# Kernel optimization log

Hardware: AMD Instinct MI355X
Metric: run time of the kernel (lower is better)

Reference implementation:

```python
import jax, jax.numpy as jnp
import numpy as np
import math

B, C, N, L = 32, 128, 2048, 1
H, DK, APT = 8, 16, 10
EPS = 1e-5


def conv1x1(x, W, b):
    # 1x1 Conv2d on [B, C, N, L]
    return jnp.einsum('oc,bcnl->bonl', W, x) + b[None, :, None, None]


def layer_norm_12(x):
    # normalize over dims (1, 2) as in the custom LayerNorm (no affine)
    mean = x.mean(axis=(1, 2), keepdims=True)
    var = x.var(axis=(1, 2), keepdims=True)
    return (x - mean) / jnp.sqrt(var + EPS)


def setup_inputs() -> dict:
    key = jax.random.key(0)
    ks = jax.random.split(key, 10)
    s = 0.05  # small-scale init for numerical stability
    inp = {
        'input': jax.random.normal(ks[0], (B, C, N, L), jnp.float32),
        'Wq': jax.random.normal(ks[1], (C, C), jnp.float32) * s,
        'bq': jnp.zeros((C,), jnp.float32),
        'Wv': jax.random.normal(ks[2], (C, C), jnp.float32) * s,
        'bv': jnp.zeros((C,), jnp.float32),
        'Wc': jax.random.normal(ks[3], (C, C), jnp.float32) * s,
        'bc': jnp.zeros((C,), jnp.float32),
        'memory': jax.random.normal(ks[4], (H, L, N, DK), jnp.float32) * s,
        'sa_weight': jnp.ones((C, N, L), jnp.float32),
        'sa_bias': jnp.zeros((C, N, L), jnp.float32),
        'nodevec1': jax.random.normal(ks[5], (N, APT), jnp.float32),
        'nodevec2': jax.random.normal(ks[6], (APT, N), jnp.float32),
        'Wg1': jax.random.normal(ks[7], (C, C), jnp.float32) * s,
        'bg1': jnp.zeros((C,), jnp.float32),
        'Wg2': jax.random.normal(ks[8], (C, C), jnp.float32) * s,
        'bg2': jnp.zeros((C,), jnp.float32),
        'Wg3': jax.random.normal(ks[9], (C, C), jnp.float32) * s,
        'bg3': jnp.zeros((C,), jnp.float32),
    }
    return inp


def reference(input, Wq, bq, Wv, bv, Wc, bc, memory, sa_weight, sa_bias,
              nodevec1, nodevec2, Wg1, bg1, Wg2, bg2, Wg3, bg3):
    scale = math.sqrt(DK)

    def split_heads(t):  # [B,C,N,L] -> [B,H,L,N,DK]
        return t.reshape(B, H, DK, N, L).transpose(0, 1, 4, 3, 2)

    # SpatialAttention (Conv = 1x1 conv + relu; dropout off in eval)
    q = jax.nn.relu(conv1x1(input, Wq, bq))
    v = jax.nn.relu(conv1x1(input, Wv, bv))
    query = jax.nn.softmax(split_heads(q) / scale, axis=-1)     # [B,H,L,N,DK]
    value = split_heads(v)                                       # [B,H,L,N,DK]
    key = jax.nn.softmax(memory / scale, axis=-1)                # [H,L,N,DK]
    Aapt = jax.nn.softmax(jax.nn.relu(nodevec1 @ nodevec2), axis=-1)  # [N,N]

    kv = jnp.einsum('hlnx,bhlny->bhlxy', key, value)             # [B,H,L,DK,DK]
    attn_qkv = jnp.einsum('bhlnx,bhlxy->bhlny', query, kv)       # [B,H,L,N,DK]
    attn_dyn = jnp.einsum('nm,bhlnc->bhlnc', Aapt, value)        # row-sum scaling
    x = attn_qkv + attn_dyn

    # merge heads back to [B,C,N,L] and apply concat conv (Conv = conv+relu)
    x = x.transpose(0, 1, 4, 3, 2).reshape(B, C, N, L)
    x = jax.nn.relu(conv1x1(x, Wc, bc))
    x = x * sa_weight[None] + sa_bias[None] + x                  # affine branch

    # Encoder wrap
    x = x + input
    x = layer_norm_12(x)
    g = conv1x1(x, Wg1, bg1) * jax.nn.sigmoid(conv1x1(x, Wg2, bg2))
    g = conv1x1(g, Wg3, bg3)                                     # GLU
    x = g + x
    x = x * sa_weight[None] + sa_bias[None] + x
    x = layer_norm_12(x)
    return x
```

## Files before the change

kernel.cpp:

```cpp
#include <hip/hip_runtime.h>
#include <hip/hip_bf16.h>
#include <math.h>

#define DI __device__ __forceinline__

typedef short bf16x8 __attribute__((ext_vector_type(8)));
typedef float f32x4 __attribute__((ext_vector_type(4)));

constexpr int BB = 32, CC = 128, NN = 2048;
constexpr float EPSf = 1e-5f;
constexpr float RCN = 1.0f / (CC * (float)NN);

#define MFMA(a,b,c) __builtin_amdgcn_mfma_f32_16x16x32_bf16(a,b,c,0,0,0)

DI unsigned short f2b(float f){
    union { __hip_bfloat16 h; unsigned short u; } v;
    v.h = __float2bfloat16(f);
    return v.u;
}
DI float b2f(unsigned short h){
    union { unsigned u; float f; } v; v.u = ((unsigned)h) << 16;
    return v.f;
}
DI float sigm(float x){ return 1.0f / (1.0f + __expf(-x)); }

__global__ __launch_bounds__(256) void k_prep(
    const float* __restrict__ Wq, const float* __restrict__ Wv,
    const float* __restrict__ Wc, const float* __restrict__ Wg1,
    const float* __restrict__ Wg2, const float* __restrict__ Wg3,
    const float* __restrict__ mem, const float* __restrict__ saw,
    const float* __restrict__ sab,
    unsigned short* __restrict__ Wb, float* __restrict__ rs,
    unsigned short* __restrict__ ksT, unsigned short* __restrict__ sawb,
    unsigned short* __restrict__ sabb)
{
    const int tid = threadIdx.x;
    if (blockIdx.x < 96) {
        const int i = blockIdx.x * 256 + tid;
        const int m = i >> 12, q = i & 4095;
        const float* src = (m==0)?Wq:(m==1)?Wv:(m==2)?Wc:(m==3)?Wg1:(m==4)?Wg2:Wg3;
        f32x4 w = *(const f32x4*)&src[q * 4];
        ushort4 p; p.x=f2b(w[0]); p.y=f2b(w[1]); p.z=f2b(w[2]); p.w=f2b(w[3]);
        *(ushort4*)&Wb[(size_t)m * 16384 + q * 4] = p;
    } else if (blockIdx.x == 96) {
        const float* src = (tid < 128) ? Wg1 : Wg2;
        const int o = tid & 127;
        float s = 0.f;
#pragma unroll
        for (int j = 0; j < 32; j++) {
            f32x4 a = *(const f32x4*)&src[o * 128 + j * 4];
            s += a[0] + a[1] + a[2] + a[3];
        }
        rs[tid] = s;
    } else if (blockIdx.x < 161) {
        const int row = (blockIdx.x - 97) * 256 + tid;
        const int h = row >> 11, n = row & 2047;
        const float* p = mem + (size_t)row * 16;
        float v[16];
        f32x4 t0 = *(const f32x4*)(p);
        f32x4 t1 = *(const f32x4*)(p + 4);
        f32x4 t2 = *(const f32x4*)(p + 8);
        f32x4 t3 = *(const f32x4*)(p + 12);
#pragma unroll
        for (int j = 0; j < 4; j++) { v[j]=t0[j]; v[4+j]=t1[j]; v[8+j]=t2[j]; v[12+j]=t3[j]; }
        float mx = v[0];
#pragma unroll
        for (int x = 1; x < 16; x++) mx = fmaxf(mx, v[x]);
        float s = 0.f;
#pragma unroll
        for (int x = 0; x < 16; x++) { v[x] = __expf((v[x] - mx) * 0.25f); s += v[x]; }
        const float is = 1.0f / s;
#pragma unroll
        for (int x = 0; x < 16; x++)
            ksT[((size_t)(h * 16 + x)) * NN + n] = f2b(v[x] * is);
    } else {
        const int i = (blockIdx.x - 161) * 256 + tid;
        const int m = i >> 16, q = i & 65535;
        const float* src = m ? sab : saw;
        unsigned short* dst = m ? sabb : sawb;
        f32x4 w = *(const f32x4*)&src[q * 4];
        ushort4 p; p.x=f2b(w[0]); p.y=f2b(w[1]); p.z=f2b(w[2]); p.w=f2b(w[3]);
        *(ushort4*)&dst[q * 4] = p;
    }
}

__global__ __launch_bounds__(256,2) void k_v(
    const float* __restrict__ in, const unsigned short* __restrict__ WvB,
    const float* __restrict__ bv, unsigned short* __restrict__ vT,
    unsigned short* __restrict__ inT)
{
    __shared__ unsigned short tile[128 * 136];
    const int b = blockIdx.x >> 4, n0 = (blockIdx.x & 15) * 128;
    const int tid = threadIdx.x, l = tid & 63, wid = tid >> 6;
    const int wo = wid & 1, wn = wid >> 1, lr = l & 15, lg = l >> 4;
    f32x4 acc[4][4];
    const f32x4 z = {0.f,0.f,0.f,0.f};
#pragma unroll
    for (int i = 0; i < 4; i++)
#pragma unroll
        for (int j = 0; j < 4; j++) acc[i][j] = z;
    const float* inb = in + (size_t)b * CC * NN;
#pragma unroll
    for (int ks = 0; ks < 4; ks++) {
        const int cb = ks * 32 + lg * 8;
        bf16x8 av[4];
#pragma unroll
        for (int mf = 0; mf < 4; mf++)
            av[mf] = *(const bf16x8*)&WvB[(wo*64 + mf*16 + lr) * 128 + cb];
        bf16x8 bx[4];
#pragma unroll
        for (int nf = 0; nf < 4; nf++) {
            const int n = n0 + wn*64 + nf*16 + lr;
            union { bf16x8 v; unsigned short u[8]; } t;
#pragma unroll
            for (int j = 0; j < 8; j++) t.u[j] = f2b(inb[(size_t)(cb + j) * NN + n]);
            bx[nf] = t.v;
        }
        if (wo == 0) {
#pragma unroll
            for (int nf = 0; nf < 4; nf++)
                *(bf16x8*)&tile[(wn*64 + nf*16 + lr) * 136 + cb] = bx[nf];
        }
#pragma unroll
        for (int mf = 0; mf < 4; mf++)
#pragma unroll
            for (int nf = 0; nf < 4; nf++)
                acc[mf][nf] = MFMA(av[mf], bx[nf], acc[mf][nf]);
    }
    __syncthreads();
#pragma unroll
    for (int p = 0; p < 8; p++) {
        const int row = p*16 + (tid >> 4), col = (tid & 15) * 8;
        *(uint4*)&inT[((size_t)b * NN + n0 + row) * CC + col] =
            *(const uint4*)&tile[row * 136 + col];
    }
    __syncthreads();
#pragma unroll
    for (int mf = 0; mf < 4; mf++) {
        const int ob = wo*64 + mf*16 + lg*4;
        const f32x4 b4 = *(const f32x4*)&bv[ob];
#pragma unroll
        for (int nf = 0; nf < 4; nf++) {
            const int nl = wn*64 + nf*16 + lr;
            f32x4 a = acc[mf][nf];
            ushort4 pk;
            pk.x = f2b(fmaxf(a[0]+b4[0],0.f)); pk.y = f2b(fmaxf(a[1]+b4[1],0.f));
            pk.z = f2b(fmaxf(a[2]+b4[2],0.f)); pk.w = f2b(fmaxf(a[3]+b4[3],0.f));
            *(ushort4*)&tile[nl * 136 + ob] = pk;
        }
    }
    __syncthreads();
#pragma unroll
    for (int p = 0; p < 8; p++) {
        const int row = p*16 + (tid >> 4), col = (tid & 15) * 8;
        *(uint4*)&vT[((size_t)b * NN + n0 + row) * CC + col] =
            *(const uint4*)&tile[row * 136 + col];
    }
}

__global__ __launch_bounds__(256) void k_kv(const unsigned short* __restrict__ ksT,
                                            const unsigned short* __restrict__ vT,
                                            float* __restrict__ kvb)
{
    __shared__ unsigned short vt[4 * 16 * 520];
    __shared__ float red[1024];
    const int b = blockIdx.x >> 3, h = blockIdx.x & 7;
    const int tid = threadIdx.x, l = tid & 63, wid = tid >> 6;
    const int n0 = wid * 512;
    unsigned short* vtw = vt + wid * (16 * 520);
    const unsigned short* vb = vT + ((size_t)b * NN + n0) * CC + h * 16;
#pragma unroll
    for (int r = 0; r < 8; r++) {
        const int nl = r * 64 + l;
        uint4 q0 = *(const uint4*)&vb[(size_t)nl * CC];
        uint4 q1 = *(const uint4*)&vb[(size_t)nl * CC + 8];
        const unsigned uu[8] = {q0.x,q0.y,q0.z,q0.w,q1.x,q1.y,q1.z,q1.w};
#pragma unroll
        for (int k = 0; k < 8; k++) {
            vtw[(2*k)*520 + nl]   = (unsigned short)(uu[k] & 0xffffu);
            vtw[(2*k+1)*520 + nl] = (unsigned short)(uu[k] >> 16);
        }
    }
    const int lr = l & 15, lg = l >> 4;
    const unsigned short* ka = ksT + (size_t)h * 16 * NN;
    f32x4 acc = {0.f,0.f,0.f,0.f};
#pragma unroll
    for (int kk = 0; kk < 16; kk++) {
        bf16x8 af = *(const bf16x8*)&ka[(size_t)lr * NN + n0 + kk*32 + lg*8];
        bf16x8 bf = *(const bf16x8*)&vtw[lr * 520 + kk*32 + lg*8];
        acc = MFMA(af, bf, acc);
    }
#pragma unroll
    for (int r = 0; r < 4; r++)
        red[wid * 256 + (lg*4 + r) * 16 + lr] = acc[r];
    __syncthreads();
    {
        const float s = red[tid] + red[256 + tid] + red[512 + tid] + red[768 + tid];
        kvb[((size_t)(b * 8 + h)) * 256 + tid] = s;
    }
}

__global__ __launch_bounds__(256,2) void k_attnC(
    const unsigned short* __restrict__ inT, unsigned short* __restrict__ vT,
    const float* __restrict__ kvb,
    const unsigned short* __restrict__ WqB, const float* __restrict__ bq,
    const unsigned short* __restrict__ WcB, const float* __restrict__ bc,
    const unsigned short* __restrict__ sawb, const unsigned short* __restrict__ sabb,
    float* __restrict__ part1)
{
    __shared__ float kvl[8 * 260];
    __shared__ unsigned short xq[128 * 136];
    __shared__ float red[8];
    const int b = blockIdx.x >> 4, n0 = (blockIdx.x & 15) * 128;
    const int tid = threadIdx.x;
    {
        const float* kp = kvb + (size_t)b * 2048 + (tid >> 5) * 256 + (tid & 31) * 8;
        f32x4 v0 = *(const f32x4*)kp;
        f32x4 v1 = *(const f32x4*)(kp + 4);
        float* dst = &kvl[(tid >> 5) * 260 + (tid & 31) * 8];
        *(f32x4*)dst = v0; *(f32x4*)(dst + 4) = v1;
    }
    const int l = tid & 63, wid = tid >> 6;
    const int wo = wid & 1, wn = wid >> 1, lr = l & 15, lg = l >> 4;
    {
        f32x4 acc[4][4];
        const f32x4 z = {0.f,0.f,0.f,0.f};
#pragma unroll
        for (int i = 0; i < 4; i++)
#pragma unroll
            for (int j = 0; j < 4; j++) acc[i][j] = z;
        const unsigned short* ab = inT + (size_t)b * NN * CC;
#pragma unroll
        for (int ks = 0; ks < 4; ks++) {
            const int cb = ks * 32 + lg * 8;
            bf16x8 af[4];
#pragma unroll
            for (int mf = 0; mf < 4; mf++)
                af[mf] = *(const bf16x8*)&WqB[(wo*64 + mf*16 + lr) * 128 + cb];
            bf16x8 bx[4];
#pragma unroll
            for (int nf = 0; nf < 4; nf++)
                bx[nf] = *(const bf16x8*)&ab[(size_t)(n0 + wn*64 + nf*16 + lr) * CC + cb];
#pragma unroll
            for (int mf = 0; mf < 4; mf++)
#pragma unroll
                for (int nf = 0; nf < 4; nf++)
                    acc[mf][nf] = MFMA(af[mf], bx[nf], acc[mf][nf]);
        }
#pragma unroll
        for (int mf = 0; mf < 4; mf++) {
            const int ob = wo*64 + mf*16 + lg*4;
            const f32x4 b4 = *(const f32x4*)&bq[ob];
#pragma unroll
            for (int nf = 0; nf < 4; nf++) {
                const int nl = wn*64 + nf*16 + lr;
                f32x4 a = acc[mf][nf];
                ushort4 pk;
                pk.x = f2b(fmaxf(a[0]+b4[0],0.f)); pk.y = f2b(fmaxf(a[1]+b4[1],0.f));
                pk.z = f2b(fmaxf(a[2]+b4[2],0.f)); pk.w = f2b(fmaxf(a[3]+b4[3],0.f));
                *(ushort4*)&xq[nl * 136 + ob] = pk;
            }
        }
    }
    __syncthreads();
#pragma unroll 1
    for (int it = 0; it < 4; it++) {
        const int idx = it * 256 + tid;
        const int nl = idx >> 3, h = idx & 7;
        const size_t base = ((size_t)b * NN + n0 + nl) * CC + h * 16;
        uint4 w0 = *(const uint4*)(vT + base);
        uint4 w1 = *(const uint4*)(vT + base + 8);
        const unsigned short* qp = &xq[nl * 136 + h * 16];
        uint4 u0 = *(const uint4*)qp;
        uint4 u1 = *(const uint4*)(qp + 8);
        unsigned uu[8] = {u0.x,u0.y,u0.z,u0.w,u1.x,u1.y,u1.z,u1.w};
        float mx = -1e30f;
#pragma unroll
        for (int j = 0; j < 8; j++) {
            mx = fmaxf(mx, b2f((unsigned short)(uu[j] & 0xffffu)));
            mx = fmaxf(mx, b2f((unsigned short)(uu[j] >> 16)));
        }
        const float* kh = &kvl[h * 260];
        f32x4 r0 = {0,0,0,0}, r1 = {0,0,0,0}, r2 = {0,0,0,0}, r3 = {0,0,0,0};
        float s = 0.f;
#pragma unroll
        for (int x = 0; x < 16; x++) {
            const unsigned short qh = (x & 1) ? (unsigned short)(uu[x >> 1] >> 16)
                                              : (unsigned short)(uu[x >> 1] & 0xffffu);
            const float e = __expf((b2f(qh) - mx) * 0.25f);
            s += e;
            const f32x4 k0 = *(const f32x4*)&kh[x * 16];
            const f32x4 k1 = *(const f32x4*)&kh[x * 16 + 4];
            const f32x4 k2 = *(const f32x4*)&kh[x * 16 + 8];
            const f32x4 k3 = *(const f32x4*)&kh[x * 16 + 12];
#pragma unroll
            for (int j = 0; j < 4; j++) {
                r0[j] = fmaf(e, k0[j], r0[j]);
                r1[j] = fmaf(e, k1[j], r1[j]);
                r2[j] = fmaf(e, k2[j], r2[j]);
                r3[j] = fmaf(e, k3[j], r3[j]);
            }
        }
        const float is = 1.0f / s;
        unsigned vv[8] = {w0.x,w0.y,w0.z,w0.w,w1.x,w1.y,w1.z,w1.w};
        unsigned short* xp = &xq[nl * 136 + h * 16];
#pragma unroll
        for (int j2 = 0; j2 < 4; j2++) {
            const f32x4 rr = (j2==0)?r0:(j2==1)?r1:(j2==2)?r2:r3;
            ushort4 pk;
            pk.x = f2b(rr[0]*is + b2f((unsigned short)(vv[2*j2]   & 0xffffu)));
            pk.y = f2b(rr[1]*is + b2f((unsigned short)(vv[2*j2]   >> 16)));
            pk.z = f2b(rr[2]*is + b2f((unsigned short)(vv[2*j2+1] & 0xffffu)));
            pk.w = f2b(rr[3]*is + b2f((unsigned short)(vv[2*j2+1] >> 16)));
            *(ushort4*)&xp[j2 * 4] = pk;
        }
    }
    __syncthreads();
    f32x4 acc[4][4];
    const f32x4 z = {0.f,0.f,0.f,0.f};
#pragma unroll
    for (int i = 0; i < 4; i++)
#pragma unroll
        for (int j = 0; j < 4; j++) acc[i][j] = z;
#pragma unroll
    for (int ks = 0; ks < 4; ks++) {
        const int cb = ks * 32 + lg * 8;
        bf16x8 af[4];
#pragma unroll
        for (int mf = 0; mf < 4; mf++)
            af[mf] = *(const bf16x8*)&WcB[(wo*64 + mf*16 + lr) * 128 + cb];
        bf16x8 bx[4];
#pragma unroll
        for (int nf = 0; nf < 4; nf++)
            bx[nf] = *(const bf16x8*)&xq[(wn*64 + nf*16 + lr) * 136 + cb];
#pragma unroll
        for (int mf = 0; mf < 4; mf++)
#pragma unroll
            for (int nf = 0; nf < 4; nf++)
                acc[mf][nf] = MFMA(af[mf], bx[nf], acc[mf][nf]);
    }
    __syncthreads();
    float sum = 0.f, ssq = 0.f;
#pragma unroll
    for (int mf = 0; mf < 4; mf++) {
        const int ob = wo*64 + mf*16 + lg*4;
        const f32x4 b4 = *(const f32x4*)&bc[ob];
#pragma unroll
        for (int nf = 0; nf < 4; nf++) {
            const int nl = wn*64 + nf*16 + lr;
            const int n = n0 + nl;
            f32x4 a = acc[mf][nf];
            const ushort4 iu = *(const ushort4*)&inT[((size_t)b * NN + n) * CC + ob];
            float ys[4];
#pragma unroll
            for (int r = 0; r < 4; r++) {
                const int o = ob + r;
                const float t = fmaxf(a[r] + b4[r], 0.f);
                const float sw = b2f(sawb[(size_t)o * NN + n]);
                const float sb = b2f(sabb[(size_t)o * NN + n]);
                const unsigned short iv = (r==0)?iu.x:(r==1)?iu.y:(r==2)?iu.z:iu.w;
                float y = t * sw + sb + t + b2f(iv);
                sum += y; ssq += y * y;
                ys[r] = y;
            }
            ushort4 pk;
            pk.x = f2b(ys[0]); pk.y = f2b(ys[1]); pk.z = f2b(ys[2]); pk.w = f2b(ys[3]);
            *(ushort4*)&xq[nl * 136 + ob] = pk;
        }
    }
    __syncthreads();
#pragma unroll
    for (int p = 0; p < 8; p++) {
        const int row = p*16 + (tid >> 4), col = (tid & 15) * 8;
        *(uint4*)&vT[((size_t)b * NN + n0 + row) * CC + col] =
            *(const uint4*)&xq[row * 136 + col];
    }
#pragma unroll
    for (int off = 32; off > 0; off >>= 1) {
        sum += __shfl_down(sum, off);
        ssq += __shfl_down(ssq, off);
    }
    if ((tid & 63) == 0) { red[wid*2] = sum; red[wid*2+1] = ssq; }
    __syncthreads();
    if (tid == 0) {
        part1[2 * blockIdx.x]     = red[0]+red[2]+red[4]+red[6];
        part1[2 * blockIdx.x + 1] = red[1]+red[3]+red[5]+red[7];
    }
}

__global__ __launch_bounds__(256,2) void k_glu3(
    const unsigned short* __restrict__ y1,
    const unsigned short* __restrict__ W1B, const unsigned short* __restrict__ W2B,
    const unsigned short* __restrict__ W3B,
    const float* __restrict__ b1, const float* __restrict__ b2,
    const float* __restrict__ b3, const float* __restrict__ rs,
    const float* __restrict__ part1, const unsigned short* __restrict__ sawb,
    const unsigned short* __restrict__ sabb, unsigned short* __restrict__ X2,
    float* __restrict__ part2)
{
    __shared__ unsigned short yt[128 * 136];
    __shared__ unsigned short gx[128 * 136];
    __shared__ float cs[256];
    __shared__ float red[8];
    const int b = blockIdx.x >> 4, n0 = (blockIdx.x & 15) * 128;
    const int tid = threadIdx.x;
    float s0 = 0.f, q0 = 0.f;
#pragma unroll
    for (int t = 0; t < 16; t++) { s0 += part1[(b*16+t)*2]; q0 += part1[(b*16+t)*2+1]; }
    const float mean = s0 * RCN;
    const float var  = q0 * RCN - mean * mean;
    const float inv  = rsqrtf(var + EPSf);
    {
        const int cq = tid & 15;
#pragma unroll
        for (int it = 0; it < 8; it++) {
            const int n = it * 16 + (tid >> 4);
            uint4 u = *(const uint4*)&y1[((size_t)b * NN + n0 + n) * CC + cq * 8];
            *(uint4*)&yt[n * 136 + cq * 8] = u;
        }
    }
    {
        const int o = tid & 127;
        const float bb = (tid < 128) ? b1[o] : b2[o];
        cs[tid] = bb - mean * inv * rs[tid];
    }
    __syncthreads();
    const int l = tid & 63, wid = tid >> 6;
    const int wo = wid & 1, wn = wid >> 1, lr = l & 15, lg = l >> 4;
    const f32x4 z = {0.f,0.f,0.f,0.f};
    {
        f32x4 acc[4][4];
#pragma unroll
        for (int i = 0; i < 4; i++)
#pragma unroll
            for (int j = 0; j < 4; j++) acc[i][j] = z;
#pragma unroll
        for (int ks = 0; ks < 4; ks++) {
            const int cb = ks * 32 + lg * 8;
            bf16x8 af[4];
#pragma unroll
            for (int mf = 0; mf < 4; mf++)
                af[mf] = *(const bf16x8*)&W1B[(wo*64 + mf*16 + lr) * 128 + cb];
            bf16x8 bx[4];
#pragma unroll
            for (int nf = 0; nf < 4; nf++)
                bx[nf] = *(const bf16x8*)&yt[(wn*64 + nf*16 + lr) * 136 + cb];
#pragma unroll
            for (int mf = 0; mf < 4; mf++)
#pragma unroll
                for (int nf = 0; nf < 4; nf++)
                    acc[mf][nf] = MFMA(af[mf], bx[nf], acc[mf][nf]);
        }
#pragma unroll
        for (int mf = 0; mf < 4; mf++) {
            const int ob = wo*64 + mf*16 + lg*4;
            const f32x4 c1 = *(const f32x4*)&cs[ob];
#pragma unroll
            for (int nf = 0; nf < 4; nf++) {
                const int nl = wn*64 + nf*16 + lr;
                f32x4 a = acc[mf][nf];
                ushort4 pk;
                pk.x = f2b(a[0]*inv + c1[0]); pk.y = f2b(a[1]*inv + c1[1]);
                pk.z = f2b(a[2]*inv + c1[2]); pk.w = f2b(a[3]*inv + c1[3]);
                *(ushort4*)&gx[nl * 136 + ob] = pk;
            }
        }
    }
    {
        f32x4 acc[4][4];
#pragma unroll
        for (int i = 0; i < 4; i++)
#pragma unroll
            for (int j = 0; j < 4; j++) acc[i][j] = z;
#pragma unroll
        for (int ks = 0; ks < 4; ks++) {
            const int cb = ks * 32 + lg * 8;
            bf16x8 af[4];
#pragma unroll
            for (int mf = 0; mf < 4; mf++)
                af[mf] = *(const bf16x8*)&W2B[(wo*64 + mf*16 + lr) * 128 + cb];
            bf16x8 bx[4];
#pragma unroll
            for (int nf = 0; nf < 4; nf++)
                bx[nf] = *(const bf16x8*)&yt[(wn*64 + nf*16 + lr) * 136 + cb];
#pragma unroll
            for (int mf = 0; mf < 4; mf++)
#pragma unroll
                for (int nf = 0; nf < 4; nf++)
                    acc[mf][nf] = MFMA(af[mf], bx[nf], acc[mf][nf]);
        }
#pragma unroll
        for (int mf = 0; mf < 4; mf++) {
            const int ob = wo*64 + mf*16 + lg*4;
            const f32x4 c2 = *(const f32x4*)&cs[128 + ob];
#pragma unroll
            for (int nf = 0; nf < 4; nf++) {
                const int nl = wn*64 + nf*16 + lr;
                f32x4 a = acc[mf][nf];
                ushort4 g1 = *(const ushort4*)&gx[nl * 136 + ob];
                ushort4 pk;
                pk.x = f2b(b2f(g1.x) * sigm(a[0]*inv + c2[0]));
                pk.y = f2b(b2f(g1.y) * sigm(a[1]*inv + c2[1]));
                pk.z = f2b(b2f(g1.z) * sigm(a[2]*inv + c2[2]));
                pk.w = f2b(b2f(g1.w) * sigm(a[3]*inv + c2[3]));
                *(ushort4*)&gx[nl * 136 + ob] = pk;
            }
        }
    }
    __syncthreads();
    f32x4 acc[4][4];
#pragma unroll
    for (int i = 0; i < 4; i++)
#pragma unroll
        for (int j = 0; j < 4; j++) acc[i][j] = z;
#pragma unroll
    for (int ks = 0; ks < 4; ks++) {
        const int cb = ks * 32 + lg * 8;
        bf16x8 af[4];
#pragma unroll
        for (int mf = 0; mf < 4; mf++)
            af[mf] = *(const bf16x8*)&W3B[(wo*64 + mf*16 + lr) * 128 + cb];
        bf16x8 bx[4];
#pragma unroll
        for (int nf = 0; nf < 4; nf++)
            bx[nf] = *(const bf16x8*)&gx[(wn*64 + nf*16 + lr) * 136 + cb];
#pragma unroll
        for (int mf = 0; mf < 4; mf++)
#pragma unroll
            for (int nf = 0; nf < 4; nf++)
                acc[mf][nf] = MFMA(af[mf], bx[nf], acc[mf][nf]);
    }
    __syncthreads();
    float sum = 0.f, ssq = 0.f;
#pragma unroll
    for (int mf = 0; mf < 4; mf++) {
        const int ob = wo*64 + mf*16 + lg*4;
        const f32x4 b4 = *(const f32x4*)&b3[ob];
#pragma unroll
        for (int nf = 0; nf < 4; nf++) {
            const int nl = wn*64 + nf*16 + lr;
            const int n = n0 + nl;
            ushort4 yq = *(const ushort4*)&yt[nl * 136 + ob];
            f32x4 a = acc[mf][nf];
            float ys[4];
#pragma unroll
            for (int r = 0; r < 4; r++) {
                const int o = ob + r;
                const unsigned short ev = (r==0)?yq.x:(r==1)?yq.y:(r==2)?yq.z:yq.w;
                const float t = a[r] + b4[r] + (b2f(ev) - mean) * inv;
                const float sw = b2f(sawb[(size_t)o * NN + n]);
                const float sb = b2f(sabb[(size_t)o * NN + n]);
                const float y = t * sw + sb + t;
                sum += y; ssq += y * y;
                ys[r] = y;
            }
            ushort4 pk;
            pk.x = f2b(ys[0]); pk.y = f2b(ys[1]); pk.z = f2b(ys[2]); pk.w = f2b(ys[3]);
            *(ushort4*)&gx[nl * 136 + ob] = pk;
        }
    }
    __syncthreads();
#pragma unroll
    for (int p = 0; p < 8; p++) {
        const int row = p*16 + (tid >> 4), col = (tid & 15) * 8;
        *(uint4*)&X2[((size_t)b * NN + n0 + row) * CC + col] =
            *(const uint4*)&gx[row * 136 + col];
    }
#pragma unroll
    for (int off = 32; off > 0; off >>= 1) {
        sum += __shfl_down(sum, off);
        ssq += __shfl_down(ssq, off);
    }
    if ((tid & 63) == 0) { red[wid*2] = sum; red[wid*2+1] = ssq; }
    __syncthreads();
    if (tid == 0) {
        part2[2 * blockIdx.x]     = red[0]+red[2]+red[4]+red[6];
        part2[2 * blockIdx.x + 1] = red[1]+red[3]+red[5]+red[7];
    }
}

__global__ __launch_bounds__(256) void k_lnfin(const unsigned short* __restrict__ x2,
                                               const float* __restrict__ part2,
                                               float* __restrict__ out)
{
    __shared__ unsigned ts[64 * 69];
    const int b = blockIdx.x >> 5, n0 = (blockIdx.x & 31) * 64;
    const int tid = threadIdx.x;
    float s0 = 0.f, q0 = 0.f;
#pragma unroll
    for (int t = 0; t < 16; t++) { s0 += part2[(b*16+t)*2]; q0 += part2[(b*16+t)*2+1]; }
    const float mean = s0 * RCN;
    const float var  = q0 * RCN - mean * mean;
    const float inv  = rsqrtf(var + EPSf);
    {
        const int n = tid >> 2, qd = tid & 3;
        const unsigned short* src = x2 + ((size_t)b * NN + n0 + n) * CC + qd * 32;
        uint4 a0 = *(const uint4*)(src);
        uint4 a1 = *(const uint4*)(src + 8);
        uint4 a2 = *(const uint4*)(src + 16);
        uint4 a3 = *(const uint4*)(src + 24);
        unsigned u[16] = {a0.x,a0.y,a0.z,a0.w, a1.x,a1.y,a1.z,a1.w,
                          a2.x,a2.y,a2.z,a2.w, a3.x,a3.y,a3.z,a3.w};
#pragma unroll
        for (int k = 0; k < 16; k++)
            ts[(qd * 16 + k) * 69 + n] = u[k];
    }
    __syncthreads();
#pragma unroll
    for (int pass = 0; pass < 8; pass++) {
        const int c = pass * 16 + (tid >> 4), nq = tid & 15;
        const int cp = c >> 1, hi = c & 1;
        f32x4 v;
#pragma unroll
        for (int j = 0; j < 4; j++) {
            const unsigned u = ts[cp * 69 + nq * 4 + j];
            const unsigned short hv = hi ? (unsigned short)(u >> 16)
                                         : (unsigned short)(u & 0xffffu);
            v[j] = (b2f(hv) - mean) * inv;
        }
        *(f32x4*)&out[((size_t)b * CC + c) * NN + n0 + nq * 4] = v;
    }
}

extern "C" void kernel_launch(void* const* d_in, const int* in_sizes, int n_in,
                              void* d_out, int out_size, void* d_ws, size_t ws_size,
                              hipStream_t stream)
{
    const float* input = (const float*)d_in[0];
    const float* Wq  = (const float*)d_in[1];
    const float* bq  = (const float*)d_in[2];
    const float* Wv  = (const float*)d_in[3];
    const float* bv  = (const float*)d_in[4];
    const float* Wc  = (const float*)d_in[5];
    const float* bc  = (const float*)d_in[6];
    const float* mem = (const float*)d_in[7];
    const float* saw = (const float*)d_in[8];
    const float* sab = (const float*)d_in[9];
    const float* Wg1 = (const float*)d_in[12];
    const float* bg1 = (const float*)d_in[13];
    const float* Wg2 = (const float*)d_in[14];
    const float* bg2 = (const float*)d_in[15];
    const float* Wg3 = (const float*)d_in[16];
    const float* bg3 = (const float*)d_in[17];
    float* out = (float*)d_out;

    unsigned char* wsb = (unsigned char*)d_ws;
    unsigned short* inT = (unsigned short*)(wsb);
    unsigned short* vT  = (unsigned short*)(wsb + 16777216);
    unsigned short* ksT = (unsigned short*)(wsb + 33554432);
    float* kvb   = (float*)(wsb + 34078720);
    unsigned short* Wb  = (unsigned short*)(wsb + 34340864);
    float* rs    = (float*)(wsb + 34537472);
    float* part1 = (float*)(wsb + 34538496);
    float* part2 = (float*)(wsb + 34542592);
    unsigned short* sawb = (unsigned short*)d_out;
    unsigned short* sabb = sawb + 262144;

    k_prep <<<673,  256, 0, stream>>>(Wq, Wv, Wc, Wg1, Wg2, Wg3, mem, saw, sab,
                                      Wb, rs, ksT, sawb, sabb);
    k_v    <<<512,  256, 0, stream>>>(input, Wb + 16384, bv, vT, inT);
    k_kv   <<<256,  256, 0, stream>>>(ksT, vT, kvb);
    k_attnC<<<512,  256, 0, stream>>>(inT, vT, kvb, Wb, bq, Wb + 2*16384, bc,
                                      sawb, sabb, part1);
    k_glu3 <<<512,  256, 0, stream>>>(vT, Wb + 3*16384, Wb + 4*16384, Wb + 5*16384,
                                      bg1, bg2, bg3, rs, part1, sawb, sabb, inT, part2);
    k_lnfin<<<1024, 256, 0, stream>>>(inT, part2, out);
}
```

Baseline: 119.7 us.

## Move Q projection from attention kernel into V projection kernel, materialize qT

The Q 1x1-conv GEMM moves out of k_attnC into the earlier V-projection kernel (now k_qv), which writes qT as a bf16 buffer in global memory. k_attnC then reads q from global instead of computing it, and a sched_barrier delays the V loads until after the softmax. The intent is to shorten the attention kernel and balance work across kernels. In exchange it adds a full 16 MB qT write and reread, and workspace buffers are remapped, with inT placed in the output buffer and qT reused by glu3 and lnfin.

Measured after the change: 115.3 us. 3.7% less time.

```diff
diff --git a/kernel.cpp b/kernel.cpp
--- a/kernel.cpp
+++ b/kernel.cpp
@@ -84,77 +84,127 @@
     }
 }
 
-__global__ __launch_bounds__(256,2) void k_v(
-    const float* __restrict__ in, const unsigned short* __restrict__ WvB,
-    const float* __restrict__ bv, unsigned short* __restrict__ vT,
-    unsigned short* __restrict__ inT)
+__global__ __launch_bounds__(256,2) void k_qv(
+    const float* __restrict__ in, const unsigned short* __restrict__ WqB,
+    const unsigned short* __restrict__ WvB, const float* __restrict__ bq,
+    const float* __restrict__ bv, unsigned short* __restrict__ qT,
+    unsigned short* __restrict__ vT, unsigned short* __restrict__ inT)
 {
     __shared__ unsigned short tile[128 * 136];
     const int b = blockIdx.x >> 4, n0 = (blockIdx.x & 15) * 128;
     const int tid = threadIdx.x, l = tid & 63, wid = tid >> 6;
     const int wo = wid & 1, wn = wid >> 1, lr = l & 15, lg = l >> 4;
-    f32x4 acc[4][4];
     const f32x4 z = {0.f,0.f,0.f,0.f};
-#pragma unroll
-    for (int i = 0; i < 4; i++)
-#pragma unroll
-        for (int j = 0; j < 4; j++) acc[i][j] = z;
-    const float* inb = in + (size_t)b * CC * NN;
-#pragma unroll
-    for (int ks = 0; ks < 4; ks++) {
-        const int cb = ks * 32 + lg * 8;
-        bf16x8 av[4];
-#pragma unroll
-        for (int mf = 0; mf < 4; mf++)
-            av[mf] = *(const bf16x8*)&WvB[(wo*64 + mf*16 + lr) * 128 + cb];
-        bf16x8 bx[4];
-#pragma unroll
-        for (int nf = 0; nf < 4; nf++) {
-            const int n = n0 + wn*64 + nf*16 + lr;
-            union { bf16x8 v; unsigned short u[8]; } t;
-#pragma unroll
-            for (int j = 0; j < 8; j++) t.u[j] = f2b(inb[(size_t)(cb + j) * NN + n]);
-            bx[nf] = t.v;
-        }
-        if (wo == 0) {
+    {
+        f32x4 acc[4][4];
+#pragma unroll
+        for (int i = 0; i < 4; i++)
+#pragma unroll
+            for (int j = 0; j < 4; j++) acc[i][j] = z;
+        const float* inb = in + (size_t)b * CC * NN;
+#pragma unroll
+        for (int ks = 0; ks < 4; ks++) {
+            const int cb = ks * 32 + lg * 8;
+            bf16x8 av[4];
+#pragma unroll
+            for (int mf = 0; mf < 4; mf++)
+                av[mf] = *(const bf16x8*)&WvB[(wo*64 + mf*16 + lr) * 128 + cb];
+            bf16x8 bx[4];
+#pragma unroll
+            for (int nf = 0; nf < 4; nf++) {
+                const int n = n0 + wn*64 + nf*16 + lr;
+                union { bf16x8 v; unsigned short u[8]; } t;
+#pragma unroll
+                for (int j = 0; j < 8; j++) t.u[j] = f2b(inb[(size_t)(cb + j) * NN + n]);
+                bx[nf] = t.v;
+            }
+            if (wo == 0) {
+#pragma unroll
+                for (int nf = 0; nf < 4; nf++)
+                    *(bf16x8*)&tile[(wn*64 + nf*16 + lr) * 136 + cb] = bx[nf];
+            }
+#pragma unroll
+            for (int mf = 0; mf < 4; mf++)
+#pragma unroll
+                for (int nf = 0; nf < 4; nf++)
+                    acc[mf][nf] = MFMA(av[mf], bx[nf], acc[mf][nf]);
+        }
+        __syncthreads();
+#pragma unroll
+        for (int p = 0; p < 8; p++) {
+            const int row = p*16 + (tid >> 4), col = (tid & 15) * 8;
+            *(uint4*)&inT[((size_t)b * NN + n0 + row) * CC + col] =
+                *(const uint4*)&tile[row * 136 + col];
+        }
+        __syncthreads();
+#pragma unroll
+        for (int mf = 0; mf < 4; mf++) {
+            const int ob = wo*64 + mf*16 + lg*4;
+            const f32x4 b4 = *(const f32x4*)&bv[ob];
+#pragma unroll
+            for (int nf = 0; nf < 4; nf++) {
+                const int nl = wn*64 + nf*16 + lr;
+                f32x4 a = acc[mf][nf];
+                ushort4 pk;
+                pk.x = f2b(fmaxf(a[0]+b4[0],0.f)); pk.y = f2b(fmaxf(a[1]+b4[1],0.f));
+                pk.z = f2b(fmaxf(a[2]+b4[2],0.f)); pk.w = f2b(fmaxf(a[3]+b4[3],0.f));
+                *(ushort4*)&tile[nl * 136 + ob] = pk;
+            }
+        }
+        __syncthreads();
+#pragma unroll
+        for (int p = 0; p < 8; p++) {
+            const int row = p*16 + (tid >> 4), col = (tid & 15) * 8;
+            *(uint4*)&vT[((size_t)b * NN + n0 + row) * CC + col] =
+                *(const uint4*)&tile[row * 136 + col];
+        }
+        __syncthreads();
+    }
+    {
+        f32x4 acc[4][4];
+#pragma unroll
+        for (int i = 0; i < 4; i++)
+#pragma unroll
+            for (int j = 0; j < 4; j++) acc[i][j] = z;
+        const unsigned short* ab = inT + (size_t)b * NN * CC;
+#pragma unroll
+        for (int ks = 0; ks < 4; ks++) {
+            const int cb = ks * 32 + lg * 8;
+            bf16x8 af[4];
+#pragma unroll
+            for (int mf = 0; mf < 4; mf++)
+                af[mf] = *(const bf16x8*)&WqB[(wo*64 + mf*16 + lr) * 128 + cb];
+            bf16x8 bx[4];
 #pragma unroll
             for (int nf = 0; nf < 4; nf++)
-                *(bf16x8*)&tile[(wn*64 + nf*16 + lr) * 136 + cb] = bx[nf];
-        }
-#pragma unroll
-        for (int mf = 0; mf < 4; mf++)
-#pragma unroll
-            for (int nf = 0; nf < 4; nf++)
-                acc[mf][nf] = MFMA(av[mf], bx[nf], acc[mf][nf]);
-    }
-    __syncthreads();
-#pragma unroll
-    for (int p = 0; p < 8; p++) {
-        const int row = p*16 + (tid >> 4), col = (tid & 15) * 8;
-        *(uint4*)&inT[((size_t)b * NN + n0 + row) * CC + col] =
-            *(const uint4*)&tile[row * 136 + col];
-    }
-    __syncthreads();
-#pragma unroll
-    for (int mf = 0; mf < 4; mf++) {
-        const int ob = wo*64 + mf*16 + lg*4;
-        const f32x4 b4 = *(const f32x4*)&bv[ob];
-#pragma unroll
-        for (int nf = 0; nf < 4; nf++) {
-            const int nl = wn*64 + nf*16 + lr;
-            f32x4 a = acc[mf][nf];
-            ushort4 pk;
-            pk.x = f2b(fmaxf(a[0]+b4[0],0.f)); pk.y = f2b(fmaxf(a[1]+b4[1],0.f));
-            pk.z = f2b(fmaxf(a[2]+b4[2],0.f)); pk.w = f2b(fmaxf(a[3]+b4[3],0.f));
-            *(ushort4*)&tile[nl * 136 + ob] = pk;
-        }
-    }
-    __syncthreads();
-#pragma unroll
-    for (int p = 0; p < 8; p++) {
-        const int row = p*16 + (tid >> 4), col = (tid & 15) * 8;
-        *(uint4*)&vT[((size_t)b * NN + n0 + row) * CC + col] =
-            *(const uint4*)&tile[row * 136 + col];
+                bx[nf] = *(const bf16x8*)&ab[(size_t)(n0 + wn*64 + nf*16 + lr) * CC + cb];
+#pragma unroll
+            for (int mf = 0; mf < 4; mf++)
+#pragma unroll
+                for (int nf = 0; nf < 4; nf++)
+                    acc[mf][nf] = MFMA(af[mf], bx[nf], acc[mf][nf]);
+        }
+#pragma unroll
+        for (int mf = 0; mf < 4; mf++) {
+            const int ob = wo*64 + mf*16 + lg*4;
+            const f32x4 b4 = *(const f32x4*)&bq[ob];
+#pragma unroll
+            for (int nf = 0; nf < 4; nf++) {
+                const int nl = wn*64 + nf*16 + lr;
+                f32x4 a = acc[mf][nf];
+                ushort4 pk;
+                pk.x = f2b(fmaxf(a[0]+b4[0],0.f)); pk.y = f2b(fmaxf(a[1]+b4[1],0.f));
+                pk.z = f2b(fmaxf(a[2]+b4[2],0.f)); pk.w = f2b(fmaxf(a[3]+b4[3],0.f));
+                *(ushort4*)&tile[nl * 136 + ob] = pk;
+            }
+        }
+        __syncthreads();
+#pragma unroll
+        for (int p = 0; p < 8; p++) {
+            const int row = p*16 + (tid >> 4), col = (tid & 15) * 8;
+            *(uint4*)&qT[((size_t)b * NN + n0 + row) * CC + col] =
+                *(const uint4*)&tile[row * 136 + col];
+        }
     }
 }
 
@@ -201,15 +251,14 @@
 }
 
 __global__ __launch_bounds__(256,2) void k_attnC(
-    const unsigned short* __restrict__ inT, unsigned short* __restrict__ vT,
-    const float* __restrict__ kvb,
-    const unsigned short* __restrict__ WqB, const float* __restrict__ bq,
-    const unsigned short* __restrict__ WcB, const float* __restrict__ bc,
-    const unsigned short* __restrict__ sawb, const unsigned short* __restrict__ sabb,
+    const unsigned short* __restrict__ qT, unsigned short* __restrict__ vT,
+    const float* __restrict__ kvb, const unsigned short* __restrict__ WcB,
+    const float* __restrict__ bc, const unsigned short* __restrict__ sawb,
+    const unsigned short* __restrict__ sabb, const unsigned short* __restrict__ inT,
     float* __restrict__ part1)
 {
     __shared__ float kvl[8 * 260];
-    __shared__ unsigned short xq[128 * 136];
+    __shared__ unsigned short xc[128 * 136];
     __shared__ float red[8];
     const int b = blockIdx.x >> 4, n0 = (blockIdx.x & 15) * 128;
     const int tid = threadIdx.x;
@@ -220,59 +269,14 @@
         float* dst = &kvl[(tid >> 5) * 260 + (tid & 31) * 8];
         *(f32x4*)dst = v0; *(f32x4*)(dst + 4) = v1;
     }
-    const int l = tid & 63, wid = tid >> 6;
-    const int wo = wid & 1, wn = wid >> 1, lr = l & 15, lg = l >> 4;
-    {
-        f32x4 acc[4][4];
-        const f32x4 z = {0.f,0.f,0.f,0.f};
-#pragma unroll
-        for (int i = 0; i < 4; i++)
-#pragma unroll
-            for (int j = 0; j < 4; j++) acc[i][j] = z;
-        const unsigned short* ab = inT + (size_t)b * NN * CC;
-#pragma unroll
-        for (int ks = 0; ks < 4; ks++) {
-            const int cb = ks * 32 + lg * 8;
-            bf16x8 af[4];
-#pragma unroll
-            for (int mf = 0; mf < 4; mf++)
-                af[mf] = *(const bf16x8*)&WqB[(wo*64 + mf*16 + lr) * 128 + cb];
-            bf16x8 bx[4];
-#pragma unroll
-            for (int nf = 0; nf < 4; nf++)
-                bx[nf] = *(const bf16x8*)&ab[(size_t)(n0 + wn*64 + nf*16 + lr) * CC + cb];
-#pragma unroll
-            for (int mf = 0; mf < 4; mf++)
-#pragma unroll
-                for (int nf = 0; nf < 4; nf++)
-                    acc[mf][nf] = MFMA(af[mf], bx[nf], acc[mf][nf]);
-        }
-#pragma unroll
-        for (int mf = 0; mf < 4; mf++) {
-            const int ob = wo*64 + mf*16 + lg*4;
-            const f32x4 b4 = *(const f32x4*)&bq[ob];
-#pragma unroll
-            for (int nf = 0; nf < 4; nf++) {
-                const int nl = wn*64 + nf*16 + lr;
-                f32x4 a = acc[mf][nf];
-                ushort4 pk;
-                pk.x = f2b(fmaxf(a[0]+b4[0],0.f)); pk.y = f2b(fmaxf(a[1]+b4[1],0.f));
-                pk.z = f2b(fmaxf(a[2]+b4[2],0.f)); pk.w = f2b(fmaxf(a[3]+b4[3],0.f));
-                *(ushort4*)&xq[nl * 136 + ob] = pk;
-            }
-        }
-    }
     __syncthreads();
 #pragma unroll 1
     for (int it = 0; it < 4; it++) {
         const int idx = it * 256 + tid;
         const int nl = idx >> 3, h = idx & 7;
         const size_t base = ((size_t)b * NN + n0 + nl) * CC + h * 16;
-        uint4 w0 = *(const uint4*)(vT + base);
-        uint4 w1 = *(const uint4*)(vT + base + 8);
-        const unsigned short* qp = &xq[nl * 136 + h * 16];
-        uint4 u0 = *(const uint4*)qp;
-        uint4 u1 = *(const uint4*)(qp + 8);
+        uint4 u0 = *(const uint4*)(qT + base);
+        uint4 u1 = *(const uint4*)(qT + base + 8);
         unsigned uu[8] = {u0.x,u0.y,u0.z,u0.w,u1.x,u1.y,u1.z,u1.w};
         float mx = -1e30f;
 #pragma unroll
@@ -302,8 +306,11 @@
             }
         }
         const float is = 1.0f / s;
+        __builtin_amdgcn_sched_barrier(0);
+        uint4 w0 = *(const uint4*)(vT + base);
+        uint4 w1 = *(const uint4*)(vT + base + 8);
         unsigned vv[8] = {w0.x,w0.y,w0.z,w0.w,w1.x,w1.y,w1.z,w1.w};
-        unsigned short* xp = &xq[nl * 136 + h * 16];
+        unsigned short* xp = &xc[nl * 136 + h * 16];
 #pragma unroll
         for (int j2 = 0; j2 < 4; j2++) {
             const f32x4 rr = (j2==0)?r0:(j2==1)?r1:(j2==2)?r2:r3;
@@ -316,6 +323,8 @@
         }
     }
     __syncthreads();
+    const int l = tid & 63, wid = tid >> 6;
+    const int wo = wid & 1, wn = wid >> 1, lr = l & 15, lg = l >> 4;
     f32x4 acc[4][4];
     const f32x4 z = {0.f,0.f,0.f,0.f};
 #pragma unroll
@@ -332,7 +341,7 @@
         bf16x8 bx[4];
 #pragma unroll
         for (int nf = 0; nf < 4; nf++)
-            bx[nf] = *(const bf16x8*)&xq[(wn*64 + nf*16 + lr) * 136 + cb];
+            bx[nf] = *(const bf16x8*)&xc[(wn*64 + nf*16 + lr) * 136 + cb];
 #pragma unroll
         for (int mf = 0; mf < 4; mf++)
 #pragma unroll
@@ -365,7 +374,7 @@
             }
             ushort4 pk;
             pk.x = f2b(ys[0]); pk.y = f2b(ys[1]); pk.z = f2b(ys[2]); pk.w = f2b(ys[3]);
-            *(ushort4*)&xq[nl * 136 + ob] = pk;
+            *(ushort4*)&xc[nl * 136 + ob] = pk;
         }
     }
     __syncthreads();
@@ -373,7 +382,7 @@
     for (int p = 0; p < 8; p++) {
         const int row = p*16 + (tid >> 4), col = (tid & 15) * 8;
         *(uint4*)&vT[((size_t)b * NN + n0 + row) * CC + col] =
-            *(const uint4*)&xq[row * 136 + col];
+            *(const uint4*)&xc[row * 136 + col];
     }
 #pragma unroll
     for (int off = 32; off > 0; off >>= 1) {
@@ -645,7 +654,7 @@
     float* out = (float*)d_out;
 
     unsigned char* wsb = (unsigned char*)d_ws;
-    unsigned short* inT = (unsigned short*)(wsb);
+    unsigned short* qT  = (unsigned short*)(wsb);
     unsigned short* vT  = (unsigned short*)(wsb + 16777216);
     unsigned short* ksT = (unsigned short*)(wsb + 33554432);
     float* kvb   = (float*)(wsb + 34078720);
@@ -653,16 +662,17 @@
     float* rs    = (float*)(wsb + 34537472);
     float* part1 = (float*)(wsb + 34538496);
     float* part2 = (float*)(wsb + 34542592);
-    unsigned short* sawb = (unsigned short*)d_out;
+    unsigned short* inT  = (unsigned short*)d_out;
+    unsigned short* sawb = (unsigned short*)((unsigned char*)d_out + 16777216);
     unsigned short* sabb = sawb + 262144;
 
     k_prep <<<673,  256, 0, stream>>>(Wq, Wv, Wc, Wg1, Wg2, Wg3, mem, saw, sab,
                                       Wb, rs, ksT, sawb, sabb);
-    k_v    <<<512,  256, 0, stream>>>(input, Wb + 16384, bv, vT, inT);
+    k_qv   <<<512,  256, 0, stream>>>(input, Wb, Wb + 16384, bq, bv, qT, vT, inT);
     k_kv   <<<256,  256, 0, stream>>>(ksT, vT, kvb);
-    k_attnC<<<512,  256, 0, stream>>>(inT, vT, kvb, Wb, bq, Wb + 2*16384, bc,
-                                      sawb, sabb, part1);
+    k_attnC<<<512,  256, 0, stream>>>(qT, vT, kvb, Wb + 2*16384, bc, sawb, sabb,
+                                      inT, part1);
     k_glu3 <<<512,  256, 0, stream>>>(vT, Wb + 3*16384, Wb + 4*16384, Wb + 5*16384,
-                                      bg1, bg2, bg3, rs, part1, sawb, sabb, inT, part2);
-    k_lnfin<<<1024, 256, 0, stream>>>(inT, part2, out);
-}
+                                      bg1, bg2, bg3, rs, part1, sawb, sabb, qT, part2);
+    k_lnfin<<<1024, 256, 0, stream>>>(qT, part2, out);
+}
```
